# Optimization experiments

Measured on AMD Instinct MI355X. Metric: run time of the kernel, lower is better.

The kernel has to match this reference:

```python
import jax, jax.numpy as jnp
import numpy as np

NUM_LAYERS = 4


def setup_inputs() -> dict:
    key = jax.random.key(0)
    k1, k2, k3, k4 = jax.random.split(key, 4)
    num_users, num_items, D, E = 100000, 50000, 64, 2000000
    N = num_users + num_items
    emb_users = jax.random.normal(k1, (num_users, D), dtype=jnp.float32)
    emb_items = jax.random.normal(k2, (num_items, D), dtype=jnp.float32)
    src = jax.random.randint(k3, (E,), 0, N, dtype=jnp.int64)
    dst = jax.random.randint(k4, (E,), 0, N, dtype=jnp.int64)
    edge_index = jnp.stack([src, dst], axis=0)
    return {"emb_users": emb_users, "emb_items": emb_items, "edge_index": edge_index}


def _lightgcn(emb_users, emb_items, edge_index):
    num_users = emb_users.shape[0]
    num_items = emb_items.shape[0]
    N = num_users + num_items
    src, dst = edge_index[0], edge_index[1]

    # gcn_norm without self-loops (PyG LGConv default): deg over destination nodes
    ones = jnp.ones(src.shape[0], dtype=emb_users.dtype)
    deg = jax.ops.segment_sum(ones, dst, num_segments=N)
    deg_inv_sqrt = jnp.where(deg > 0, jax.lax.rsqrt(jnp.maximum(deg, 1.0)), 0.0)
    norm = deg_inv_sqrt[src] * deg_inv_sqrt[dst]  # [E]

    emb = jnp.concatenate([emb_users, emb_items], axis=0)  # [N, D]
    acc = emb
    for _ in range(NUM_LAYERS):
        msg = norm[:, None] * emb[src]  # [E, D]
        emb = jax.ops.segment_sum(msg, dst, num_segments=N)
        acc = acc + emb

    # original: 1/(L+1) * mean(stack, dim=1) == sum / (L+1)^2
    emb_final = acc / float((NUM_LAYERS + 1) ** 2)
    return emb_final[:num_users], emb_final[num_users:]


def reference(emb_users, emb_items, edge_index):
    return _lightgcn(emb_users, emb_items, edge_index)
```

## Files before the change

kernel.cpp:

```cpp
#include <hip/hip_runtime.h>
#include <hip/hip_bf16.h>

#define D 64
#define NUM_LAYERS 4
#define TILE 4096
#define EPT 16
#define BKMAX 320


__device__ __forceinline__ float bf_lo(unsigned u) { return __uint_as_float(u << 16); }
__device__ __forceinline__ float bf_hi(unsigned u) { return __uint_as_float(u & 0xffff0000u); }
__device__ __forceinline__ unsigned bf_pack(float x, float y) {
    __hip_bfloat16 bx = __float2bfloat16(x);
    __hip_bfloat16 by = __float2bfloat16(y);
    return (unsigned)(*reinterpret_cast<unsigned short*>(&bx))
         | ((unsigned)(*reinterpret_cast<unsigned short*>(&by)) << 16);
}


__global__ void bhist_kernel(const int* __restrict__ dst, int* __restrict__ bcnt,
                             int* __restrict__ deg, int E, int nbk) {
    __shared__ int h[BKMAX];
    for (int i = threadIdx.x; i < nbk; i += blockDim.x) h[i] = 0;
    __syncthreads();
    int stride = gridDim.x * blockDim.x;
    int gid = blockIdx.x * blockDim.x + threadIdx.x;
    int E4 = (((size_t)dst & 15) == 0) ? (E >> 2) : 0;
    const int4* dst4 = (const int4*)dst;
    for (int i = gid; i < E4; i += stride) {
        int4 d = dst4[i];
        atomicAdd(&h[d.x >> 9], 1); atomicAdd(&deg[d.x], 1);
        atomicAdd(&h[d.y >> 9], 1); atomicAdd(&deg[d.y], 1);
        atomicAdd(&h[d.z >> 9], 1); atomicAdd(&deg[d.z], 1);
        atomicAdd(&h[d.w >> 9], 1); atomicAdd(&deg[d.w], 1);
    }
    for (int e = (E4 << 2) + gid; e < E; e += stride) {
        int d = dst[e];
        atomicAdd(&h[d >> 9], 1); atomicAdd(&deg[d], 1);
    }
    __syncthreads();
    for (int i = threadIdx.x; i < nbk; i += blockDim.x)
        if (h[i] > 0) atomicAdd(&bcnt[i], h[i]);
}

__global__ __launch_bounds__(512) void bscan_kernel(const int* __restrict__ bcnt,
                                                    int* __restrict__ bstart,
                                                    int* __restrict__ gcur, int nbk, int E) {
    __shared__ int sm[512];
    int t = threadIdx.x;
    int v = (t < nbk) ? bcnt[t] : 0;
    sm[t] = v;
    __syncthreads();
    for (int ofs = 1; ofs < 512; ofs <<= 1) {
        int x = (t >= ofs) ? sm[t - ofs] : 0;
        __syncthreads();
        sm[t] += x;
        __syncthreads();
    }
    int excl = sm[t] - v;
    if (t < nbk) { bstart[t] = excl; gcur[t] = excl; }
    if (t == 0) bstart[nbk] = E;
}


__global__ __launch_bounds__(256) void placeA_kernel(const int* __restrict__ src,
                                                     const int* __restrict__ dst,
                                                     int* __restrict__ gcur,
                                                     int* __restrict__ mid,
                                                     int E, int nbk) {
    __shared__ int hist[BKMAX];
    __shared__ int gbase[BKMAX];
    int t = threadIdx.x;
    int tile0 = blockIdx.x * TILE;
    for (int i = t; i < nbk; i += 256) hist[i] = 0;
    __syncthreads();

    bool al = (((size_t)src & 15) == 0) && (((size_t)dst & 15) == 0);

    int p_[EPT];
    int b_[EPT];
    int r_[EPT];
#pragma unroll
    for (int i4 = 0; i4 < 4; ++i4) {
        int e0 = tile0 + i4 * 1024 + t * 4;
        int4 s4, d4;
        if (al && (e0 + 3 < E)) {
            s4 = *(const int4*)(src + e0);
            d4 = *(const int4*)(dst + e0);
        } else {
            s4 = make_int4(0, 0, 0, 0); d4 = make_int4(0, 0, 0, 0);
            if (e0     < E) { s4.x = src[e0];     d4.x = dst[e0]; }
            if (e0 + 1 < E) { s4.y = src[e0 + 1]; d4.y = dst[e0 + 1]; }
            if (e0 + 2 < E) { s4.z = src[e0 + 2]; d4.z = dst[e0 + 2]; }
            if (e0 + 3 < E) { s4.w = src[e0 + 3]; d4.w = dst[e0 + 3]; }
        }
        int ss[4] = { s4.x, s4.y, s4.z, s4.w };
        int dd[4] = { d4.x, d4.y, d4.z, d4.w };
#pragma unroll
        for (int k = 0; k < 4; ++k) {
            int i = i4 * 4 + k;
            int e = e0 + k;
            b_[i] = -1;
            if (e < E) {
                p_[i] = ss[k] | ((dd[k] & 511) << 18);
                b_[i] = dd[k] >> 9;
                r_[i] = atomicAdd(&hist[b_[i]], 1);
            }
        }
    }
    __syncthreads();
    for (int b = t; b < nbk; b += 256) {
        int h = hist[b];
        gbase[b] = (h > 0) ? atomicAdd(&gcur[b], h) : 0;
    }
    __syncthreads();
#pragma unroll
    for (int i = 0; i < EPT; ++i) {
        if (b_[i] >= 0) mid[gbase[b_[i]] + r_[i]] = p_[i];
    }
}

__global__ __launch_bounds__(512) void placeB_kernel(const int* __restrict__ bstart,
                                                     const int* __restrict__ mid,
                                                     const int* __restrict__ deg,
                                                     int* __restrict__ row_start,
                                                     int2* __restrict__ csr,
                                                     int N, int nbk, int E) {
    __shared__ int sc[512];
    __shared__ int cur[512];
    __shared__ float dloc[512];
    int b = blockIdx.x;
    int t = threadIdx.x;
    int node0 = b << 9;
    int node = node0 + t;
    int lo = bstart[b], hi = bstart[b + 1];
    int d = (node < N) ? deg[node] : 0;
    sc[t] = d;
    __syncthreads();
    for (int ofs = 1; ofs < 512; ofs <<= 1) {
        int x = (t >= ofs) ? sc[t - ofs] : 0;
        __syncthreads();
        sc[t] += x;
        __syncthreads();
    }
    int excl = sc[t] - d;
    if (node < N) row_start[node] = lo + excl;
    cur[t] = lo + excl;
    dloc[t] = (d > 0) ? rsqrtf((float)d) : 0.0f;
    if (b == nbk - 1 && t == 0) row_start[N] = E;
    __syncthreads();
    for (int e = lo + t; e < hi; e += 512) {
        int m = mid[e];
        int l = (m >> 18) & 511;
        int s = m & 0x3FFFF;
        int dsv = deg[s];
        float w = ((dsv > 0) ? rsqrtf((float)dsv) : 0.0f) * dloc[l];
        int slot = atomicAdd(&cur[l], 1);
        csr[slot] = make_int2(s, __float_as_int(w));
    }
}


__global__ void init_kernel(const float* __restrict__ users, const float* __restrict__ items,
                            unsigned* __restrict__ A, int nu_elems, int total8) {
    int i = blockIdx.x * blockDim.x + threadIdx.x;
    if (i >= total8) return;
    long long base = (long long)i * 8;
    const float4* p;
    if (base < nu_elems) p = (const float4*)users + (base >> 2);
    else                 p = (const float4*)items + ((base - nu_elems) >> 2);
    float4 a = p[0];
    float4 b = p[1];
    uint4 r;
    r.x = bf_pack(a.x, a.y);
    r.y = bf_pack(a.z, a.w);
    r.z = bf_pack(b.x, b.y);
    r.w = bf_pack(b.z, b.w);
    ((uint4*)A)[i] = r;
}

template <int FINAL>
__global__ void gather_kernel(const int* __restrict__ row_start,
                              const int2* __restrict__ csr,
                              const uint2* __restrict__ Au,
                              uint2* __restrict__ Bu,
                              const float* __restrict__ users, const float* __restrict__ items,
                              const uint2* __restrict__ L1u, const uint2* __restrict__ L2u,
                              float* __restrict__ out,
                              int N, int nu) {
    int node = (blockIdx.x * blockDim.x + threadIdx.x) >> 6;
    if (node >= N) return;
    int lane = threadIdx.x & 63;
    int q = lane >> 4;
    int c = lane & 15;
    int beg = row_start[node];
    int end = row_start[node + 1];
    int deg = end - beg;
    float ax = 0.0f, ay = 0.0f, az = 0.0f, aw = 0.0f;

    for (int base = 0; base < deg; base += 64) {
        int chunk = min(64, deg - base);
        int   sl = 0;
        float wl = 0.0f;
        if (lane < chunk) {
            int2 e = csr[beg + base + lane];
            sl = e.x;
            wl = __int_as_float(e.y);
        }
        int k = 0;
        for (; k + 8 <= chunk; k += 8) {
            int i0 = k + q, i1 = k + 4 + q;
            int   s0 = __shfl(sl, i0), s1 = __shfl(sl, i1);
            float w0 = __shfl(wl, i0), w1 = __shfl(wl, i1);
            uint2 u0 = Au[(size_t)s0 * 16 + c];
            uint2 u1 = Au[(size_t)s1 * 16 + c];
            ax += w0 * bf_lo(u0.x); ay += w0 * bf_hi(u0.x);
            az += w0 * bf_lo(u0.y); aw += w0 * bf_hi(u0.y);
            ax += w1 * bf_lo(u1.x); ay += w1 * bf_hi(u1.x);
            az += w1 * bf_lo(u1.y); aw += w1 * bf_hi(u1.y);
        }
        for (; k < chunk; k += 4) {
            int i0 = k + q;
            int   s = __shfl(sl, i0);
            float w = __shfl(wl, i0);
            uint2 u = Au[(size_t)s * 16 + c];
            ax += w * bf_lo(u.x); ay += w * bf_hi(u.x);
            az += w * bf_lo(u.y); aw += w * bf_hi(u.y);
        }
    }

    ax += __shfl_xor(ax, 16); ay += __shfl_xor(ay, 16);
    az += __shfl_xor(az, 16); aw += __shfl_xor(aw, 16);
    ax += __shfl_xor(ax, 32); ay += __shfl_xor(ay, 32);
    az += __shfl_xor(az, 32); aw += __shfl_xor(aw, 32);

    if (q == 0) {
        size_t ro = (size_t)node * 16 + c;
        if (FINAL) {
            uint2 l1 = L1u[ro], l2 = L2u[ro], l3 = Au[ro];
            float4 e0;
            if (node < nu) e0 = ((const float4*)users)[ro];
            else           e0 = ((const float4*)items)[(size_t)(node - nu) * 16 + c];
            float rx = (e0.x + bf_lo(l1.x) + bf_lo(l2.x) + bf_lo(l3.x) + ax) * 0.04f;
            float ry = (e0.y + bf_hi(l1.x) + bf_hi(l2.x) + bf_hi(l3.x) + ay) * 0.04f;
            float rz = (e0.z + bf_lo(l1.y) + bf_lo(l2.y) + bf_lo(l3.y) + az) * 0.04f;
            float rw = (e0.w + bf_hi(l1.y) + bf_hi(l2.y) + bf_hi(l3.y) + aw) * 0.04f;
            ((float4*)out)[ro] = make_float4(rx, ry, rz, rw);
        } else {
            uint2 p;
            p.x = bf_pack(ax, ay);
            p.y = bf_pack(az, aw);
            Bu[ro] = p;
        }
    }
}


extern "C" void kernel_launch(void* const* d_in, const int* in_sizes, int n_in,
                              void* d_out, int out_size, void* d_ws, size_t ws_size,
                              hipStream_t stream) {
    const float* users = (const float*)d_in[0];
    const float* items = (const float*)d_in[1];
    const int*   eidx  = (const int*)d_in[2];

    const int nu = in_sizes[0] / D;
    const int ni = in_sizes[1] / D;
    const int N  = nu + ni;
    const int E  = in_sizes[2] / 2;
    const int Nf = N * D;
    const int nbk = (N + 511) >> 9;

    const int* src = eidx;
    const int* dst = eidx + E;

    char* ws = (char*)d_ws;
    size_t off = 0;
    auto alloc = [&](size_t bytes) {
        char* p = ws + off;
        off += (bytes + 255) & ~(size_t)255;
        return p;
    };
    int*   row_start = (int*)alloc((size_t)(N + 1) * 4);
    int*   bcnt      = (int*)alloc(BKMAX * 4 + (size_t)N * 4);
    int*   deg       = bcnt + BKMAX;
    int*   bstart    = (int*)alloc((BKMAX + 1) * 4);
    int*   gcur      = (int*)alloc(BKMAX * 4);
    int2*  csr       = (int2*)alloc((size_t)E * 8);
    unsigned* A0 = (unsigned*)alloc((size_t)Nf * 2);
    unsigned* L1 = (unsigned*)alloc((size_t)Nf * 2);
    unsigned* L2 = (unsigned*)alloc((size_t)Nf * 2);
    unsigned* L3 = (unsigned*)alloc((size_t)Nf * 2);
    int* mid = (int*)L3;

    const int B256 = 256;
    auto blocks = [](long long n, int b) { return (int)((n + b - 1) / b); };

    hipMemsetAsync(bcnt, 0, BKMAX * 4 + (size_t)N * 4, stream);
    bhist_kernel<<<1024, B256, 0, stream>>>(dst, bcnt, deg, E, nbk);
    bscan_kernel<<<1, 512, 0, stream>>>(bcnt, bstart, gcur, nbk, E);

    placeA_kernel<<<blocks(E, TILE), B256, 0, stream>>>(src, dst, gcur, mid, E, nbk);
    placeB_kernel<<<nbk, 512, 0, stream>>>(bstart, mid, deg, row_start, csr, N, nbk, E);

    init_kernel<<<blocks(Nf / 8, B256), B256, 0, stream>>>(users, items, A0, nu * D, Nf / 8);

    const int ggrid = blocks(N, B256 / 64);
    gather_kernel<0><<<ggrid, B256, 0, stream>>>(row_start, csr, (const uint2*)A0, (uint2*)L1,
                                                 nullptr, nullptr, nullptr, nullptr, nullptr, N, nu);
    gather_kernel<0><<<ggrid, B256, 0, stream>>>(row_start, csr, (const uint2*)L1, (uint2*)L2,
                                                 nullptr, nullptr, nullptr, nullptr, nullptr, N, nu);
    gather_kernel<0><<<ggrid, B256, 0, stream>>>(row_start, csr, (const uint2*)L2, (uint2*)L3,
                                                 nullptr, nullptr, nullptr, nullptr, nullptr, N, nu);
    gather_kernel<1><<<ggrid, B256, 0, stream>>>(row_start, csr, (const uint2*)L3, nullptr,
                                                 users, items, (const uint2*)L1, (const uint2*)L2,
                                                 (float*)d_out, N, nu);
}
```

Measured before the change: 462.2 us.

## Compute degrees per bucket in shared memory instead of global atomics

```diff
diff --git a/kernel.cpp b/kernel.cpp
--- a/kernel.cpp
+++ b/kernel.cpp
@@ -18,8 +18,7 @@
 }
 
 
-__global__ void bhist_kernel(const int* __restrict__ dst, int* __restrict__ bcnt,
-                             int* __restrict__ deg, int E, int nbk) {
+__global__ void bhist_kernel(const int* __restrict__ dst, int* __restrict__ bcnt, int E, int nbk) {
     __shared__ int h[BKMAX];
     for (int i = threadIdx.x; i < nbk; i += blockDim.x) h[i] = 0;
     __syncthreads();
@@ -29,15 +28,13 @@
     const int4* dst4 = (const int4*)dst;
     for (int i = gid; i < E4; i += stride) {
         int4 d = dst4[i];
-        atomicAdd(&h[d.x >> 9], 1); atomicAdd(&deg[d.x], 1);
-        atomicAdd(&h[d.y >> 9], 1); atomicAdd(&deg[d.y], 1);
-        atomicAdd(&h[d.z >> 9], 1); atomicAdd(&deg[d.z], 1);
-        atomicAdd(&h[d.w >> 9], 1); atomicAdd(&deg[d.w], 1);
-    }
-    for (int e = (E4 << 2) + gid; e < E; e += stride) {
-        int d = dst[e];
-        atomicAdd(&h[d >> 9], 1); atomicAdd(&deg[d], 1);
-    }
+        atomicAdd(&h[d.x >> 9], 1);
+        atomicAdd(&h[d.y >> 9], 1);
+        atomicAdd(&h[d.z >> 9], 1);
+        atomicAdd(&h[d.w >> 9], 1);
+    }
+    for (int e = (E4 << 2) + gid; e < E; e += stride)
+        atomicAdd(&h[dst[e] >> 9], 1);
     __syncthreads();
     for (int i = threadIdx.x; i < nbk; i += blockDim.x)
         if (h[i] > 0) atomicAdd(&bcnt[i], h[i]);
@@ -120,41 +117,60 @@
     }
 }
 
-__global__ __launch_bounds__(512) void placeB_kernel(const int* __restrict__ bstart,
-                                                     const int* __restrict__ mid,
-                                                     const int* __restrict__ deg,
-                                                     int* __restrict__ row_start,
-                                                     int2* __restrict__ csr,
-                                                     int N, int nbk, int E) {
+__global__ __launch_bounds__(512) void placeB1_kernel(const int* __restrict__ bstart,
+                                                      const int* __restrict__ mid,
+                                                      int* __restrict__ row_start,
+                                                      float* __restrict__ dis,
+                                                      int N, int nbk, int E) {
+    __shared__ int degsm[512];
     __shared__ int sc[512];
+    int b = blockIdx.x;
+    int t = threadIdx.x;
+    int node0 = b << 9;
+    int lo = bstart[b], hi = bstart[b + 1];
+    degsm[t] = 0;
+    __syncthreads();
+    for (int e = lo + t; e < hi; e += 512)
+        atomicAdd(&degsm[(mid[e] >> 18) & 511], 1);
+    __syncthreads();
+    int d = degsm[t];
+    sc[t] = d;
+    __syncthreads();
+    for (int ofs = 1; ofs < 512; ofs <<= 1) {
+        int x = (t >= ofs) ? sc[t - ofs] : 0;
+        __syncthreads();
+        sc[t] += x;
+        __syncthreads();
+    }
+    int excl = sc[t] - d;
+    int node = node0 + t;
+    if (node < N) {
+        row_start[node] = lo + excl;
+        dis[node] = (d > 0) ? rsqrtf((float)d) : 0.0f;
+    }
+    if (b == nbk - 1 && t == 0) row_start[N] = E;
+}
+
+__global__ __launch_bounds__(512) void placeB2_kernel(const int* __restrict__ bstart,
+                                                      const int* __restrict__ mid,
+                                                      const int* __restrict__ row_start,
+                                                      const float* __restrict__ dis,
+                                                      int2* __restrict__ csr, int N) {
     __shared__ int cur[512];
     __shared__ float dloc[512];
     int b = blockIdx.x;
     int t = threadIdx.x;
     int node0 = b << 9;
     int node = node0 + t;
+    if (node < N) { cur[t] = row_start[node]; dloc[t] = dis[node]; }
+    else          { cur[t] = 0; dloc[t] = 0.0f; }
+    __syncthreads();
     int lo = bstart[b], hi = bstart[b + 1];
-    int d = (node < N) ? deg[node] : 0;
-    sc[t] = d;
-    __syncthreads();
-    for (int ofs = 1; ofs < 512; ofs <<= 1) {
-        int x = (t >= ofs) ? sc[t - ofs] : 0;
-        __syncthreads();
-        sc[t] += x;
-        __syncthreads();
-    }
-    int excl = sc[t] - d;
-    if (node < N) row_start[node] = lo + excl;
-    cur[t] = lo + excl;
-    dloc[t] = (d > 0) ? rsqrtf((float)d) : 0.0f;
-    if (b == nbk - 1 && t == 0) row_start[N] = E;
-    __syncthreads();
     for (int e = lo + t; e < hi; e += 512) {
         int m = mid[e];
         int l = (m >> 18) & 511;
         int s = m & 0x3FFFF;
-        int dsv = deg[s];
-        float w = ((dsv > 0) ? rsqrtf((float)dsv) : 0.0f) * dloc[l];
+        float w = dis[s] * dloc[l];
         int slot = atomicAdd(&cur[l], 1);
         csr[slot] = make_int2(s, __float_as_int(w));
     }
@@ -203,9 +219,9 @@
         int   sl = 0;
         float wl = 0.0f;
         if (lane < chunk) {
-            int2 e = csr[beg + base + lane];
-            sl = e.x;
-            wl = __int_as_float(e.y);
+            long long p = __builtin_nontemporal_load((const long long*)(csr + beg + base + lane));
+            sl = (int)(p & 0xFFFFFFFFLL);
+            wl = __int_as_float((int)(p >> 32));
         }
         int k = 0;
         for (; k + 8 <= chunk; k += 8) {
@@ -237,7 +253,13 @@
     if (q == 0) {
         size_t ro = (size_t)node * 16 + c;
         if (FINAL) {
-            uint2 l1 = L1u[ro], l2 = L2u[ro], l3 = Au[ro];
+            uint2 l1;
+            l1.x = __builtin_nontemporal_load(&L1u[ro].x);
+            l1.y = __builtin_nontemporal_load(&L1u[ro].y);
+            uint2 l2;
+            l2.x = __builtin_nontemporal_load(&L2u[ro].x);
+            l2.y = __builtin_nontemporal_load(&L2u[ro].y);
+            uint2 l3 = Au[ro];
             float4 e0;
             if (node < nu) e0 = ((const float4*)users)[ro];
             else           e0 = ((const float4*)items)[(size_t)(node - nu) * 16 + c];
@@ -280,9 +302,9 @@
         off += (bytes + 255) & ~(size_t)255;
         return p;
     };
+    float* dis       = (float*)alloc((size_t)N * 4);
     int*   row_start = (int*)alloc((size_t)(N + 1) * 4);
-    int*   bcnt      = (int*)alloc(BKMAX * 4 + (size_t)N * 4);
-    int*   deg       = bcnt + BKMAX;
+    int*   bcnt      = (int*)alloc(BKMAX * 4);
     int*   bstart    = (int*)alloc((BKMAX + 1) * 4);
     int*   gcur      = (int*)alloc(BKMAX * 4);
     int2*  csr       = (int2*)alloc((size_t)E * 8);
@@ -295,12 +317,13 @@
     const int B256 = 256;
     auto blocks = [](long long n, int b) { return (int)((n + b - 1) / b); };
 
-    hipMemsetAsync(bcnt, 0, BKMAX * 4 + (size_t)N * 4, stream);
-    bhist_kernel<<<1024, B256, 0, stream>>>(dst, bcnt, deg, E, nbk);
+    hipMemsetAsync(bcnt, 0, BKMAX * 4, stream);
+    bhist_kernel<<<1024, B256, 0, stream>>>(dst, bcnt, E, nbk);
     bscan_kernel<<<1, 512, 0, stream>>>(bcnt, bstart, gcur, nbk, E);
 
     placeA_kernel<<<blocks(E, TILE), B256, 0, stream>>>(src, dst, gcur, mid, E, nbk);
-    placeB_kernel<<<nbk, 512, 0, stream>>>(bstart, mid, deg, row_start, csr, N, nbk, E);
+    placeB1_kernel<<<nbk, 512, 0, stream>>>(bstart, mid, row_start, dis, N, nbk, E);
+    placeB2_kernel<<<nbk, 512, 0, stream>>>(bstart, mid, row_start, dis, csr, N);
 
     init_kernel<<<blocks(Nf / 8, B256), B256, 0, stream>>>(users, items, A0, nu * D, Nf / 8);
 
```

After: 419.3 us. 9.3% less time.
